# Kernel tuning notes

Measured on AMD Instinct MI355X. Metric: run time of the kernel, lower is better.

Reference implementation:

```python
import jax, jax.numpy as jnp
import numpy as np

FG_THRESH = 0.5   # cfg.TRAIN.FG_THRESH
BG_THRESH = 0.1   # cfg.TRAIN.BG_THRESH
EPS = 1e-9
N_STREAMS = 4

def _area(b):
    return (b[..., 2] - b[..., 0] + 1.0) * (b[..., 3] - b[..., 1] + 1.0)

def _pairwise_iou(bb, gt):
    # bb [R,4], gt [G,4] -> [R,G] pascal IoU (with +1)
    x1 = jnp.maximum(bb[:, None, 0], gt[None, :, 0])
    y1 = jnp.maximum(bb[:, None, 1], gt[None, :, 1])
    x2 = jnp.minimum(bb[:, None, 2], gt[None, :, 2])
    y2 = jnp.minimum(bb[:, None, 3], gt[None, :, 3])
    iw = jnp.maximum(x2 - x1 + 1.0, 0.0)
    ih = jnp.maximum(y2 - y1 + 1.0, 0.0)
    inter = iw * ih
    return inter / (_area(bb)[:, None] + _area(gt)[None, :] - inter)

def _iou_vs_one(boxes, bm):
    # boxes [4,4] vs single box bm [4] -> mutual iou [4]
    x1 = jnp.maximum(boxes[:, 0], bm[0])
    y1 = jnp.maximum(boxes[:, 1], bm[1])
    x2 = jnp.minimum(boxes[:, 2], bm[2])
    y2 = jnp.minimum(boxes[:, 3], bm[3])
    iw = jnp.maximum(x2 - x1 + 1.0, 0.0)
    ih = jnp.maximum(y2 - y1 + 1.0, 0.0)
    inter = iw * ih
    return inter / (_area(boxes) + _area(bm) - inter)

def _select_per_class(boxes, present):
    # boxes [4,4] top proposals of the 4 streams for one class; present: bool
    # Faithful port of the instance_selector while-loop (at most 4 iterations).
    area = _area(boxes)
    active = jnp.full((N_STREAMS,), present)
    selected = jnp.zeros((N_STREAMS,), bool)
    idx = jnp.arange(N_STREAMS)
    for _ in range(N_STREAMS):
        m = jnp.argmax(jnp.where(active, area, -jnp.inf))
        bm = boxes[m]
        iou = _iou_vs_one(boxes, bm)
        enclosed = ((boxes[:, 0] > bm[0]) & (boxes[:, 1] > bm[1]) &
                    (boxes[:, 2] < bm[2]) & (boxes[:, 3] < bm[3]))
        pick = active & (idx == m)                      # max-area pick
        keep = active & (iou < 0.1) & (~enclosed)        # kept as extra gt
        selected = selected | pick | keep
        # removed: high-overlap (>0.3, includes m itself), enclosed, kept
        active = active & ~((iou > 0.3) | enclosed | keep)
    return selected

def instance_selector(cls_probs, rois, im_labels):
    # cls_probs [4,R,C], rois [R,4], im_labels [1,C]
    top_idx = jnp.argmax(cls_probs, axis=1)                      # [4,C]
    top_boxes = rois[top_idx]                                    # [4,C,4]
    top_scores = jnp.take_along_axis(cls_probs, top_idx[:, None, :], axis=1)[:, 0, :]  # [4,C]
    boxes_c = jnp.transpose(top_boxes, (1, 0, 2))                # [C,4,4]
    scores_c = top_scores.T                                      # [C,4]
    present = im_labels[0] > 0                                   # [C]
    selected = jax.vmap(_select_per_class)(boxes_c, present)     # [C,4]
    C = scores_c.shape[0]
    gt_boxes = boxes_c.reshape(-1, 4)                            # [4C,4]
    gt_scores = scores_c.reshape(-1)                             # [4C]
    gt_classes = jnp.repeat(jnp.arange(1, C + 1), N_STREAMS)     # [4C]
    return gt_boxes, gt_classes, gt_scores, selected.reshape(-1)

def pcl_loss(rois, cls_prob_new, gt_boxes, gt_classes, gt_scores, valid):
    R = rois.shape[0]
    G = gt_boxes.shape[0]
    ov = _pairwise_iou(rois, gt_boxes)                   # [R,G]
    ov = jnp.where(valid[None, :], ov, -1.0)             # mask unselected gts
    assign = jnp.argmax(ov, axis=1)
    maxov = jnp.max(ov, axis=1)
    lab = gt_classes[assign]
    w = gt_scores[assign]
    bg = maxov < FG_THRESH
    lab = jnp.where(bg, 0, lab)
    assign = jnp.where(bg, -1, assign)
    w = jnp.where(maxov < BG_THRESH, 0.0, w)
    p = jnp.clip(cls_prob_new, EPS, 1.0 - EPS)
    prob_a = p[jnp.arange(R), lab]                       # prob at assigned class
    fg = (assign >= 0).astype(p.dtype)
    seg = jnp.where(assign >= 0, assign, G)              # dummy bucket G
    sums = jax.ops.segment_sum(prob_a * fg, seg, num_segments=G + 1)[:G]
    counts = jax.ops.segment_sum(fg, seg, num_segments=G + 1)[:G]
    mean_prob = sums / jnp.maximum(counts, 1.0)
    mean_safe = jnp.where(counts > 0, mean_prob, 1.0)
    pos = -jnp.sum(jnp.where(valid & (counts > 0),
                             jnp.log(mean_safe) * counts * gt_scores, 0.0))
    n_mask = jnp.where(lab == 0, w, 0.0)
    neg = -jnp.sum(jnp.log(p[:, 0]) * n_mask)
    return (pos + neg) / max(800, R)

def setup_inputs() -> dict:
    key = jax.random.key(0)
    ks = jax.random.split(key, 10)
    R, C, W, H = 100000, 20, 1000.0, 1000.0
    cx = jax.random.uniform(ks[0], (R,)) * (W - 100.0) + 50.0
    cy = jax.random.uniform(ks[1], (R,)) * (H - 100.0) + 50.0
    bw = jax.random.uniform(ks[2], (R,)) * 400.0 + 16.0
    bh = jax.random.uniform(ks[3], (R,)) * 400.0 + 16.0
    x1 = jnp.clip(cx - bw / 2, 0.0, W - 2.0)
    y1 = jnp.clip(cy - bh / 2, 0.0, H - 2.0)
    x2 = jnp.maximum(jnp.minimum(cx + bw / 2, W - 1.0), x1 + 1.0)
    y2 = jnp.maximum(jnp.minimum(cy + bh / 2, H - 1.0), y1 + 1.0)
    rois = jnp.stack([x1, y1, x2, y2], axis=1).astype(jnp.float32)
    cls0 = jax.random.uniform(ks[4], (R, C), dtype=jnp.float32)
    cls1 = jax.random.uniform(ks[5], (R, C), dtype=jnp.float32)
    cls2 = jax.random.uniform(ks[6], (R, C), dtype=jnp.float32)
    cls3 = jax.random.uniform(ks[7], (R, C), dtype=jnp.float32)
    cls_prob_new = jax.nn.softmax(jax.random.normal(ks[8], (R, C + 1), dtype=jnp.float32), axis=1)
    im_labels = (jax.random.uniform(ks[9], (1, C)) < 0.15).astype(jnp.int32)
    im_labels = im_labels.at[0, 0].set(1)  # ensure at least one positive class
    return {"rois": rois, "cls0_prob": cls0, "cls1_prob": cls1,
            "cls2_prob": cls2, "cls3_prob": cls3,
            "cls_prob_new": cls_prob_new, "im_labels": im_labels}

def reference(rois, cls0_prob, cls1_prob, cls2_prob, cls3_prob, cls_prob_new, im_labels):
    cls_probs = jnp.stack([cls0_prob, cls1_prob, cls2_prob, cls3_prob])  # [4,R,C]
    gtb, gtc, gts, valid = instance_selector(cls_probs, rois, im_labels)
    loss = pcl_loss(rois, cls_prob_new, gtb, gtc, gts, valid)
    return loss, gtb, gts, valid
```

## Files before the change

### kernel.cpp

```cpp
#include <hip/hip_runtime.h>
#include <cfloat>
#include <climits>
#include <math.h>

#define NSTREAM 4
#define NCLS    20
#define NGT     (NSTREAM * NCLS)
#define TPB     256
#define TPB_B   320
#define ROWS_PER_CHUNK 256
#define CHUNKS  2
#define ROWS_PER_BLOCK (ROWS_PER_CHUNK * CHUNKS)
#define PADW    21

#define WS_PV    0
#define WS_PI    16000
#define WS_GTB   32000
#define WS_GTS   32320
#define WS_VALID 32400
#define WS_SUMS  32480
#define WS_CNTS  32560
#define WS_NEG   32640
#define WS_NV    32641
#define WS_GLIST 32642

__global__ __launch_bounds__(TPB) void argmax_kernel(
    const float* __restrict__ c0, const float* __restrict__ c1,
    const float* __restrict__ c2, const float* __restrict__ c3,
    float* __restrict__ pv, int* __restrict__ pi, int R, int xblk)
{
    __shared__ float stage[ROWS_PER_CHUNK * PADW];
    __shared__ float sv[NCLS][4];
    __shared__ int   si[NCLS][4];

    const int s   = blockIdx.y;
    const int xb  = blockIdx.x;
    const float* cls = (s == 0) ? c0 : (s == 1) ? c1 : (s == 2) ? c2 : c3;
    const int tid  = threadIdx.x;
    const int lane = tid & 63;
    const int wv   = tid >> 6;

    float bv[NCLS];
    int   bi_[NCLS];
#pragma unroll
    for (int c = 0; c < NCLS; ++c) { bv[c] = -FLT_MAX; bi_[c] = INT_MAX; }

    const int r0b = xb * ROWS_PER_BLOCK;
    for (int k = 0; k < CHUNKS; ++k) {
        const int r0 = r0b + k * ROWS_PER_CHUNK;
        int rows = R - r0;
        if (rows > ROWS_PER_CHUNK) rows = ROWS_PER_CHUNK;

        if (rows > 0) {
            const float4* src = reinterpret_cast<const float4*>(cls + (size_t)r0 * NCLS);
            const int nf4 = rows * (NCLS / 4);
#pragma unroll
            for (int j = 0; j < 5; ++j) {
                const int f = tid + j * TPB;
                if (f < nf4) {
                    float4 v = src[f];
                    const int w   = 4 * f;
                    const int row = w / NCLS;
                    const int col = w - row * NCLS;
                    float* d = &stage[row * PADW + col];
                    d[0] = v.x; d[1] = v.y; d[2] = v.z; d[3] = v.w;
                }
            }
        }
        __syncthreads();
        if (rows > 0 && tid < rows) {
            const int gidx = r0 + tid;
            const float* rowp = &stage[tid * PADW];
#pragma unroll
            for (int c = 0; c < NCLS; ++c) {
                float v = rowp[c];
                if (v > bv[c]) { bv[c] = v; bi_[c] = gidx; }
            }
        }
        __syncthreads();
    }

#pragma unroll
    for (int off = 32; off > 0; off >>= 1) {
#pragma unroll
        for (int c = 0; c < NCLS; ++c) {
            float ov = __shfl_down(bv[c], off);
            int   oi = __shfl_down(bi_[c], off);
            if (ov > bv[c] || (ov == bv[c] && oi < bi_[c])) { bv[c] = ov; bi_[c] = oi; }
        }
    }
    if (lane == 0) {
#pragma unroll
        for (int c = 0; c < NCLS; ++c) { sv[c][wv] = bv[c]; si[c][wv] = bi_[c]; }
    }
    __syncthreads();
    if (tid < NCLS) {
        float best = sv[tid][0]; int bidx = si[tid][0];
#pragma unroll
        for (int w = 1; w < 4; ++w) {
            float v = sv[tid][w]; int i = si[tid][w];
            if (v > best || (v == best && i < bidx)) { best = v; bidx = i; }
        }
        const int p = s * NCLS + tid;
        pv[(size_t)p * xblk + xb] = best;
        pi[(size_t)p * xblk + xb] = bidx;
    }
}

__global__ __launch_bounds__(TPB_B) void select_kernel(
    const float* __restrict__ rois,
    const int* __restrict__ imlab,
    float* ws, float* __restrict__ d_out, int xblk)
{
    const float* pv   = ws + WS_PV;
    const int*   pi   = (const int*)(ws + WS_PI);
    float* gtb   = ws + WS_GTB;
    float* gts   = ws + WS_GTS;
    int*   valid = (int*)(ws + WS_VALID);
    float* sums  = ws + WS_SUMS;
    float* cnts  = ws + WS_CNTS;
    int*   nvp   = (int*)(ws + WS_NV);
    int*   glist = (int*)(ws + WS_GLIST);

    const int tid = threadIdx.x;
    __shared__ float s_pv4[4][NGT];
    __shared__ int   s_pi4[4][NGT];
    __shared__ float s_box[NGT][4];

    {
        const int q = tid / NGT;
        const int p = tid % NGT;
        const int chunk = (xblk + 3) >> 2;
        const int b0 = q * chunk;
        int b1 = b0 + chunk; if (b1 > xblk) b1 = xblk;
        float best = -FLT_MAX; int bidx = INT_MAX;
        for (int b = b0; b < b1; ++b) {
            float v = pv[(size_t)p * xblk + b];
            int   i = pi[(size_t)p * xblk + b];
            if (v > best || (v == best && i < bidx)) { best = v; bidx = i; }
        }
        s_pv4[q][p] = best; s_pi4[q][p] = bidx;
    }
    __syncthreads();

    if (tid < NGT) {
        float best = s_pv4[0][tid]; int bidx = s_pi4[0][tid];
#pragma unroll
        for (int q = 1; q < 4; ++q) {
            float v = s_pv4[q][tid]; int i = s_pi4[q][tid];
            if (v > best || (v == best && i < bidx)) { best = v; bidx = i; }
        }
        const int st = tid / NCLS;
        const int c  = tid % NCLS;
        const int g  = c * NSTREAM + st;
        float4 box = reinterpret_cast<const float4*>(rois)[bidx];
        s_box[g][0] = box.x; s_box[g][1] = box.y;
        s_box[g][2] = box.z; s_box[g][3] = box.w;
        gtb[g * 4 + 0] = box.x; gtb[g * 4 + 1] = box.y;
        gtb[g * 4 + 2] = box.z; gtb[g * 4 + 3] = box.w;
        gts[g] = best;
        d_out[1 + g * 4 + 0] = box.x; d_out[1 + g * 4 + 1] = box.y;
        d_out[1 + g * 4 + 2] = box.z; d_out[1 + g * 4 + 3] = box.w;
        d_out[1 + NGT * 4 + g] = best;
        sums[g] = 0.0f; cnts[g] = 0.0f;
    }
    if (tid == 0) ws[WS_NEG] = 0.0f;
    __syncthreads();

    if (tid < NCLS) {
        const int c = tid;
        const bool present = imlab[c] > 0;
        float bx[NSTREAM][4], area[NSTREAM];
#pragma unroll
        for (int s = 0; s < NSTREAM; ++s) {
#pragma unroll
            for (int k = 0; k < 4; ++k) bx[s][k] = s_box[c * NSTREAM + s][k];
            area[s] = (bx[s][2] - bx[s][0] + 1.0f) * (bx[s][3] - bx[s][1] + 1.0f);
        }
        bool active[NSTREAM], sel[NSTREAM];
#pragma unroll
        for (int s = 0; s < NSTREAM; ++s) { active[s] = present; sel[s] = false; }

        for (int it = 0; it < NSTREAM; ++it) {
            int m = 0; float best = -FLT_MAX;
#pragma unroll
            for (int s = 0; s < NSTREAM; ++s) {
                float v = active[s] ? area[s] : -FLT_MAX;
                if (v > best) { best = v; m = s; }
            }
            const float bmx1 = bx[m][0], bmy1 = bx[m][1];
            const float bmx2 = bx[m][2], bmy2 = bx[m][3];
            const float am = area[m];
            bool nact[NSTREAM];
#pragma unroll
            for (int s = 0; s < NSTREAM; ++s) {
                float x1 = fmaxf(bx[s][0], bmx1), y1 = fmaxf(bx[s][1], bmy1);
                float x2 = fminf(bx[s][2], bmx2), y2 = fminf(bx[s][3], bmy2);
                float iw = fmaxf(x2 - x1 + 1.0f, 0.0f), ih = fmaxf(y2 - y1 + 1.0f, 0.0f);
                float inter = iw * ih;
                float iou = inter / (area[s] + am - inter);
                bool enclosed = (bx[s][0] > bmx1) && (bx[s][1] > bmy1) &&
                                (bx[s][2] < bmx2) && (bx[s][3] < bmy2);
                bool pick = active[s] && (s == m);
                bool keep = active[s] && (iou < 0.1f) && (!enclosed);
                sel[s] = sel[s] || pick || keep;
                nact[s] = active[s] && !((iou > 0.3f) || enclosed || keep);
            }
#pragma unroll
            for (int s = 0; s < NSTREAM; ++s) active[s] = nact[s];
        }
#pragma unroll
        for (int s = 0; s < NSTREAM; ++s) {
            const int g = c * NSTREAM + s;
            valid[g] = sel[s] ? 1 : 0;
            d_out[1 + NGT * 4 + NGT + g] = sel[s] ? 1.0f : 0.0f;
        }
    }
    __syncthreads();

    if (tid == 0) {
        int nv = 0;
        for (int g = 0; g < NGT; ++g) if (valid[g]) glist[nv++] = g;
        nvp[0] = nv;
    }
}

__global__ __launch_bounds__(TPB) void assign_kernel(
    const float* __restrict__ rois, const float* __restrict__ clsnew,
    float* ws, int R)
{
    const float* gtb  = ws + WS_GTB;
    const float* gts  = ws + WS_GTS;
    float* sums = ws + WS_SUMS;
    float* cnts = ws + WS_CNTS;
    float* negp = ws + WS_NEG;
    const int* nvp   = (const int*)(ws + WS_NV);
    const int* glist = (const int*)(ws + WS_GLIST);

    __shared__ float4 s_gt[NGT];
    __shared__ float  s_ga[NGT];
    __shared__ float  s_gs[NGT];
    __shared__ int    s_lab[NGT];
    __shared__ int    s_gidx[NGT];
    __shared__ float  s_sum[NGT];
    __shared__ float  s_cnt[NGT];
    __shared__ float  s_neg;
    __shared__ int    s_nv;

    const int tid = threadIdx.x;
    if (tid == 0) { s_neg = 0.0f; s_nv = nvp[0]; }
    if (tid < NGT) { s_sum[tid] = 0.0f; s_cnt[tid] = 0.0f; }
    __syncthreads();
    const int nv = s_nv;
    if (tid < nv) {
        const int g = glist[tid];
        float4 b = reinterpret_cast<const float4*>(gtb)[g];
        s_gt[tid] = b;
        s_ga[tid] = (b.z - b.x + 1.0f) * (b.w - b.y + 1.0f);
        s_gs[tid] = gts[g];
        s_lab[tid] = g / NSTREAM + 1;
        s_gidx[tid] = g;
    }
    __syncthreads();

    const int r = blockIdx.x * TPB + tid;
    if (r < R) {
        float4 bb = reinterpret_cast<const float4*>(rois)[r];
        float ab = (bb.z - bb.x + 1.0f) * (bb.w - bb.y + 1.0f);
        float best = -FLT_MAX; int bestj = 0;
        for (int j = 0; j < nv; ++j) {
            float4 gt = s_gt[j];
            float x1 = fmaxf(bb.x, gt.x), y1 = fmaxf(bb.y, gt.y);
            float x2 = fminf(bb.z, gt.z), y2 = fminf(bb.w, gt.w);
            float iw = fmaxf(x2 - x1 + 1.0f, 0.0f), ih = fmaxf(y2 - y1 + 1.0f, 0.0f);
            float inter = iw * ih;
            float v = inter / (ab + s_ga[j] - inter);
            if (v > best) { best = v; bestj = j; }
        }
        if (best >= 0.5f) {
            const int lab = s_lab[bestj];
            float pa = clsnew[(size_t)r * (NCLS + 1) + lab];
            pa = fminf(fmaxf(pa, 1e-9f), 1.0f - 1e-9f);
            atomicAdd(&s_sum[bestj], pa);
            atomicAdd(&s_cnt[bestj], 1.0f);
        } else if (best >= 0.1f) {
            float p0 = clsnew[(size_t)r * (NCLS + 1)];
            p0 = fminf(fmaxf(p0, 1e-9f), 1.0f - 1e-9f);
            atomicAdd(&s_neg, logf(p0) * s_gs[bestj]);
        }
    }
    __syncthreads();

    if (tid < nv && s_cnt[tid] != 0.0f) {
        atomicAdd(&sums[s_gidx[tid]], s_sum[tid]);
        atomicAdd(&cnts[s_gidx[tid]], s_cnt[tid]);
    }
    if (tid == 0 && s_neg != 0.0f) atomicAdd(negp, s_neg);
}

__global__ __launch_bounds__(128) void finalize_kernel(
    float* ws, float* __restrict__ d_out, int R)
{
    const float* sums  = ws + WS_SUMS;
    const float* cnts  = ws + WS_CNTS;
    const float* gts   = ws + WS_GTS;
    const int*   valid = (const int*)(ws + WS_VALID);
    const float* negp  = ws + WS_NEG;

    __shared__ float s_wred[2];
    const int tid = threadIdx.x;
    const int lane = tid & 63;
    float t = 0.0f;
    if (tid < NGT) {
        float cnt = cnts[tid];
        if (valid[tid] && cnt > 0.0f)
            t = logf(sums[tid] / cnt) * cnt * gts[tid];
    }
#pragma unroll
    for (int off = 32; off > 0; off >>= 1) t += __shfl_down(t, off);
    if (lane == 0) s_wred[tid >> 6] = t;
    __syncthreads();
    if (tid == 0) {
        float pos = -(s_wred[0] + s_wred[1]);
        float neg = -negp[0];
        d_out[0] = (pos + neg) / fmaxf(800.0f, (float)R);
    }
}

extern "C" void kernel_launch(void* const* d_in, const int* in_sizes, int n_in,
                              void* d_out, int out_size, void* d_ws, size_t ws_size,
                              hipStream_t stream) {
    const float* rois   = (const float*)d_in[0];
    const float* c0     = (const float*)d_in[1];
    const float* c1     = (const float*)d_in[2];
    const float* c2     = (const float*)d_in[3];
    const float* c3     = (const float*)d_in[4];
    const float* clsnew = (const float*)d_in[5];
    const int*   imlab  = (const int*)d_in[6];
    const int R = in_sizes[0] / 4;

    float* ws  = (float*)d_ws;
    float* out = (float*)d_out;
    float* pv  = ws + WS_PV;
    int*   pi  = (int*)(ws + WS_PI);

    const int xblk = (R + ROWS_PER_BLOCK - 1) / ROWS_PER_BLOCK;

    argmax_kernel<<<dim3(xblk, NSTREAM), TPB, 0, stream>>>(c0, c1, c2, c3, pv, pi, R, xblk);
    select_kernel<<<1, TPB_B, 0, stream>>>(rois, imlab, ws, out, xblk);
    assign_kernel<<<(R + TPB - 1) / TPB, TPB, 0, stream>>>(rois, clsnew, ws, R);
    finalize_kernel<<<1, 128, 0, stream>>>(ws, out, R);
}
```

Before: 154.5 us.

## Fuse select and finalize into preceding kernels via last-block ticket counters

Replaces the separate single-block select and finalize kernels with last-block-done patterns: each grid atomically increments a ticket in workspace, and the final block runs the cross-block reduction and selection (or the loss finalize) inline. A small init kernel zeroes accumulators and tickets, so there are three launches instead of four. This is meant to cut launch gaps and serial single-block kernels, at the cost of threadfences, a serial xblk reduction by 80 threads in one block, and an extra tiny init launch.

```diff
diff --git a/kernel.cpp b/kernel.cpp
--- a/kernel.cpp
+++ b/kernel.cpp
@@ -7,7 +7,6 @@
 #define NCLS    20
 #define NGT     (NSTREAM * NCLS)
 #define TPB     256
-#define TPB_B   320
 #define ROWS_PER_CHUNK 256
 #define CHUNKS  2
 #define ROWS_PER_BLOCK (ROWS_PER_CHUNK * CHUNKS)
@@ -23,15 +22,34 @@
 #define WS_NEG   32640
 #define WS_NV    32641
 #define WS_GLIST 32642
-
-__global__ __launch_bounds__(TPB) void argmax_kernel(
+#define WS_TK1   32722
+#define WS_TK2   32723
+
+__global__ __launch_bounds__(128) void init_kernel(float* ws)
+{
+    const int t = threadIdx.x;
+    if (t < NGT) { ws[WS_SUMS + t] = 0.0f; ws[WS_CNTS + t] = 0.0f; }
+    if (t == 0) {
+        ws[WS_NEG] = 0.0f;
+        ((int*)ws)[WS_TK1] = 0;
+        ((int*)ws)[WS_TK2] = 0;
+    }
+}
+
+__global__ __launch_bounds__(TPB) void argmax_select_kernel(
     const float* __restrict__ c0, const float* __restrict__ c1,
     const float* __restrict__ c2, const float* __restrict__ c3,
-    float* __restrict__ pv, int* __restrict__ pi, int R, int xblk)
+    const float* __restrict__ rois, const int* __restrict__ imlab,
+    float* ws, float* __restrict__ d_out, int R, int xblk)
 {
     __shared__ float stage[ROWS_PER_CHUNK * PADW];
     __shared__ float sv[NCLS][4];
     __shared__ int   si[NCLS][4];
+    __shared__ float s_box[NGT][4];
+    __shared__ int   s_last;
+
+    float* pv = ws + WS_PV;
+    int*   pi = (int*)(ws + WS_PI);
 
     const int s   = blockIdx.y;
     const int xb  = blockIdx.x;
@@ -105,50 +123,30 @@
         pv[(size_t)p * xblk + xb] = best;
         pi[(size_t)p * xblk + xb] = bidx;
     }
-}
-
-__global__ __launch_bounds__(TPB_B) void select_kernel(
-    const float* __restrict__ rois,
-    const int* __restrict__ imlab,
-    float* ws, float* __restrict__ d_out, int xblk)
-{
-    const float* pv   = ws + WS_PV;
-    const int*   pi   = (const int*)(ws + WS_PI);
+
+    __threadfence();
+    __syncthreads();
+    if (tid == 0) {
+        int old = atomicAdd((int*)ws + WS_TK1, 1);
+        s_last = (old == xblk * NSTREAM - 1) ? 1 : 0;
+    }
+    __syncthreads();
+    if (!s_last) return;
+    __threadfence();
+
     float* gtb   = ws + WS_GTB;
     float* gts   = ws + WS_GTS;
     int*   valid = (int*)(ws + WS_VALID);
-    float* sums  = ws + WS_SUMS;
-    float* cnts  = ws + WS_CNTS;
     int*   nvp   = (int*)(ws + WS_NV);
     int*   glist = (int*)(ws + WS_GLIST);
 
-    const int tid = threadIdx.x;
-    __shared__ float s_pv4[4][NGT];
-    __shared__ int   s_pi4[4][NGT];
-    __shared__ float s_box[NGT][4];
-
-    {
-        const int q = tid / NGT;
-        const int p = tid % NGT;
-        const int chunk = (xblk + 3) >> 2;
-        const int b0 = q * chunk;
-        int b1 = b0 + chunk; if (b1 > xblk) b1 = xblk;
+    if (tid < NGT) {
+        const float* v  = pv + (size_t)tid * xblk;
+        const int*   ii = pi + (size_t)tid * xblk;
         float best = -FLT_MAX; int bidx = INT_MAX;
-        for (int b = b0; b < b1; ++b) {
-            float v = pv[(size_t)p * xblk + b];
-            int   i = pi[(size_t)p * xblk + b];
-            if (v > best || (v == best && i < bidx)) { best = v; bidx = i; }
-        }
-        s_pv4[q][p] = best; s_pi4[q][p] = bidx;
-    }
-    __syncthreads();
-
-    if (tid < NGT) {
-        float best = s_pv4[0][tid]; int bidx = s_pi4[0][tid];
-#pragma unroll
-        for (int q = 1; q < 4; ++q) {
-            float v = s_pv4[q][tid]; int i = s_pi4[q][tid];
-            if (v > best || (v == best && i < bidx)) { best = v; bidx = i; }
+        for (int b = 0; b < xblk; ++b) {
+            float val = v[b]; int idx = ii[b];
+            if (val > best || (val == best && idx < bidx)) { best = val; bidx = idx; }
         }
         const int st = tid / NCLS;
         const int c  = tid % NCLS;
@@ -162,9 +160,7 @@
         d_out[1 + g * 4 + 0] = box.x; d_out[1 + g * 4 + 1] = box.y;
         d_out[1 + g * 4 + 2] = box.z; d_out[1 + g * 4 + 3] = box.w;
         d_out[1 + NGT * 4 + g] = best;
-        sums[g] = 0.0f; cnts[g] = 0.0f;
-    }
-    if (tid == 0) ws[WS_NEG] = 0.0f;
+    }
     __syncthreads();
 
     if (tid < NCLS) {
@@ -172,48 +168,48 @@
         const bool present = imlab[c] > 0;
         float bx[NSTREAM][4], area[NSTREAM];
 #pragma unroll
-        for (int s = 0; s < NSTREAM; ++s) {
-#pragma unroll
-            for (int k = 0; k < 4; ++k) bx[s][k] = s_box[c * NSTREAM + s][k];
-            area[s] = (bx[s][2] - bx[s][0] + 1.0f) * (bx[s][3] - bx[s][1] + 1.0f);
+        for (int s2 = 0; s2 < NSTREAM; ++s2) {
+#pragma unroll
+            for (int k = 0; k < 4; ++k) bx[s2][k] = s_box[c * NSTREAM + s2][k];
+            area[s2] = (bx[s2][2] - bx[s2][0] + 1.0f) * (bx[s2][3] - bx[s2][1] + 1.0f);
         }
         bool active[NSTREAM], sel[NSTREAM];
 #pragma unroll
-        for (int s = 0; s < NSTREAM; ++s) { active[s] = present; sel[s] = false; }
+        for (int s2 = 0; s2 < NSTREAM; ++s2) { active[s2] = present; sel[s2] = false; }
 
         for (int it = 0; it < NSTREAM; ++it) {
             int m = 0; float best = -FLT_MAX;
 #pragma unroll
-            for (int s = 0; s < NSTREAM; ++s) {
-                float v = active[s] ? area[s] : -FLT_MAX;
-                if (v > best) { best = v; m = s; }
+            for (int s2 = 0; s2 < NSTREAM; ++s2) {
+                float v = active[s2] ? area[s2] : -FLT_MAX;
+                if (v > best) { best = v; m = s2; }
             }
             const float bmx1 = bx[m][0], bmy1 = bx[m][1];
             const float bmx2 = bx[m][2], bmy2 = bx[m][3];
             const float am = area[m];
             bool nact[NSTREAM];
 #pragma unroll
-            for (int s = 0; s < NSTREAM; ++s) {
-                float x1 = fmaxf(bx[s][0], bmx1), y1 = fmaxf(bx[s][1], bmy1);
-                float x2 = fminf(bx[s][2], bmx2), y2 = fminf(bx[s][3], bmy2);
+            for (int s2 = 0; s2 < NSTREAM; ++s2) {
+                float x1 = fmaxf(bx[s2][0], bmx1), y1 = fmaxf(bx[s2][1], bmy1);
+                float x2 = fminf(bx[s2][2], bmx2), y2 = fminf(bx[s2][3], bmy2);
                 float iw = fmaxf(x2 - x1 + 1.0f, 0.0f), ih = fmaxf(y2 - y1 + 1.0f, 0.0f);
                 float inter = iw * ih;
-                float iou = inter / (area[s] + am - inter);
-                bool enclosed = (bx[s][0] > bmx1) && (bx[s][1] > bmy1) &&
-                                (bx[s][2] < bmx2) && (bx[s][3] < bmy2);
-                bool pick = active[s] && (s == m);
-                bool keep = active[s] && (iou < 0.1f) && (!enclosed);
-                sel[s] = sel[s] || pick || keep;
-                nact[s] = active[s] && !((iou > 0.3f) || enclosed || keep);
+                float iou = inter / (area[s2] + am - inter);
+                bool enclosed = (bx[s2][0] > bmx1) && (bx[s2][1] > bmy1) &&
+                                (bx[s2][2] < bmx2) && (bx[s2][3] < bmy2);
+                bool pick = active[s2] && (s2 == m);
+                bool keep = active[s2] && (iou < 0.1f) && (!enclosed);
+                sel[s2] = sel[s2] || pick || keep;
+                nact[s2] = active[s2] && !((iou > 0.3f) || enclosed || keep);
             }
 #pragma unroll
-            for (int s = 0; s < NSTREAM; ++s) active[s] = nact[s];
-        }
-#pragma unroll
-        for (int s = 0; s < NSTREAM; ++s) {
-            const int g = c * NSTREAM + s;
-            valid[g] = sel[s] ? 1 : 0;
-            d_out[1 + NGT * 4 + NGT + g] = sel[s] ? 1.0f : 0.0f;
+            for (int s2 = 0; s2 < NSTREAM; ++s2) active[s2] = nact[s2];
+        }
+#pragma unroll
+        for (int s2 = 0; s2 < NSTREAM; ++s2) {
+            const int g = c * NSTREAM + s2;
+            valid[g] = sel[s2] ? 1 : 0;
+            d_out[1 + NGT * 4 + NGT + g] = sel[s2] ? 1.0f : 0.0f;
         }
     }
     __syncthreads();
@@ -225,9 +221,9 @@
     }
 }
 
-__global__ __launch_bounds__(TPB) void assign_kernel(
+__global__ __launch_bounds__(TPB) void assign_finalize_kernel(
     const float* __restrict__ rois, const float* __restrict__ clsnew,
-    float* ws, int R)
+    float* ws, float* __restrict__ d_out, int R)
 {
     const float* gtb  = ws + WS_GTB;
     const float* gts  = ws + WS_GTS;
@@ -236,6 +232,7 @@
     float* negp = ws + WS_NEG;
     const int* nvp   = (const int*)(ws + WS_NV);
     const int* glist = (const int*)(ws + WS_GLIST);
+    const int* valid = (const int*)(ws + WS_VALID);
 
     __shared__ float4 s_gt[NGT];
     __shared__ float  s_ga[NGT];
@@ -246,8 +243,13 @@
     __shared__ float  s_cnt[NGT];
     __shared__ float  s_neg;
     __shared__ int    s_nv;
-
-    const int tid = threadIdx.x;
+    __shared__ int    s_last;
+    __shared__ float  s_wred[4];
+
+    const int tid  = threadIdx.x;
+    const int lane = tid & 63;
+    const int wv   = tid >> 6;
+
     if (tid == 0) { s_neg = 0.0f; s_nv = nvp[0]; }
     if (tid < NGT) { s_sum[tid] = 0.0f; s_cnt[tid] = 0.0f; }
     __syncthreads();
@@ -296,20 +298,17 @@
         atomicAdd(&cnts[s_gidx[tid]], s_cnt[tid]);
     }
     if (tid == 0 && s_neg != 0.0f) atomicAdd(negp, s_neg);
-}
-
-__global__ __launch_bounds__(128) void finalize_kernel(
-    float* ws, float* __restrict__ d_out, int R)
-{
-    const float* sums  = ws + WS_SUMS;
-    const float* cnts  = ws + WS_CNTS;
-    const float* gts   = ws + WS_GTS;
-    const int*   valid = (const int*)(ws + WS_VALID);
-    const float* negp  = ws + WS_NEG;
-
-    __shared__ float s_wred[2];
-    const int tid = threadIdx.x;
-    const int lane = tid & 63;
+
+    __threadfence();
+    __syncthreads();
+    if (tid == 0) {
+        int old = atomicAdd((int*)ws + WS_TK2, 1);
+        s_last = (old == (int)gridDim.x - 1) ? 1 : 0;
+    }
+    __syncthreads();
+    if (!s_last) return;
+    __threadfence();
+
     float t = 0.0f;
     if (tid < NGT) {
         float cnt = cnts[tid];
@@ -318,10 +317,10 @@
     }
 #pragma unroll
     for (int off = 32; off > 0; off >>= 1) t += __shfl_down(t, off);
-    if (lane == 0) s_wred[tid >> 6] = t;
+    if (lane == 0) s_wred[wv] = t;
     __syncthreads();
     if (tid == 0) {
-        float pos = -(s_wred[0] + s_wred[1]);
+        float pos = -(s_wred[0] + s_wred[1] + s_wred[2] + s_wred[3]);
         float neg = -negp[0];
         d_out[0] = (pos + neg) / fmaxf(800.0f, (float)R);
     }
@@ -341,13 +340,12 @@
 
     float* ws  = (float*)d_ws;
     float* out = (float*)d_out;
-    float* pv  = ws + WS_PV;
-    int*   pi  = (int*)(ws + WS_PI);
 
     const int xblk = (R + ROWS_PER_BLOCK - 1) / ROWS_PER_BLOCK;
 
-    argmax_kernel<<<dim3(xblk, NSTREAM), TPB, 0, stream>>>(c0, c1, c2, c3, pv, pi, R, xblk);
-    select_kernel<<<1, TPB_B, 0, stream>>>(rois, imlab, ws, out, xblk);
-    assign_kernel<<<(R + TPB - 1) / TPB, TPB, 0, stream>>>(rois, clsnew, ws, R);
-    finalize_kernel<<<1, 128, 0, stream>>>(ws, out, R);
+    init_kernel<<<1, 128, 0, stream>>>(ws);
+    argmax_select_kernel<<<dim3(xblk, NSTREAM), TPB, 0, stream>>>(
+        c0, c1, c2, c3, rois, imlab, ws, out, R, xblk);
+    assign_finalize_kernel<<<(R + TPB - 1) / TPB, TPB, 0, stream>>>(
+        rois, clsnew, ws, out, R);
 }
```

Measured after the change: 247.8 us. 1.6x slower.
